# Kernel optimization log

Hardware: AMD Instinct MI355X
Metric: run time of the kernel (lower is better)

Reference implementation:

```python
import jax, jax.numpy as jnp
import numpy as np


def setup_inputs() -> dict:
    key = jax.random.key(0)
    kq, kk, kv = jax.random.split(key, 3)
    N, L, H, D = 2, 2048, 16, 64
    Q = jax.random.normal(kq, (N, L, H, D), dtype=jnp.float32)
    K = jax.random.normal(kk, (N, L, H, D), dtype=jnp.float32)
    V = jax.random.normal(kv, (N, L, H, D), dtype=jnp.float32)
    return {"Q": Q, "K": K, "V": V}


def reference(Q, K, V):
    # Q: [N, l_q, H, d], K: [N, l_k, H, d], V: [N, l_k, H, d_v]
    d_key = K.shape[-1]
    scale = 1.0 / jnp.sqrt(jnp.asarray(d_key, dtype=Q.dtype))
    # scores: [N, l_q, l_k, H] (matches torch sum over d, softmax over l_k)
    scores = jnp.einsum("nqhd,nkhd->nqkh", Q, K) * scale
    attn = jax.nn.softmax(scores, axis=2)
    # out: [N, l_q, H, d_v]
    out = jnp.einsum("nqkh,nkhd->nqhd", attn, V)
    return out
```

## Files before the change

kernel.cpp:

```cpp
#include <hip/hip_runtime.h>
#include <hip/hip_bf16.h>

typedef __attribute__((ext_vector_type(8))) short bf16x8;
typedef __attribute__((ext_vector_type(4))) float float4_t;
typedef __attribute__((ext_vector_type(2))) float f32x2;
typedef __attribute__((ext_vector_type(16))) float f32x16;
typedef __attribute__((ext_vector_type(4))) int int4v;
typedef __attribute__((ext_vector_type(2))) int int2v;

constexpr int Lseq = 2048;
constexpr int ROWS = 1024;
constexpr float SCALE_LOG2E = 0.18033688011112042f;

__device__ short g_Kb[32 * 32 * 4096];
__device__ short g_Vb[32 * 32 * 4096];

__device__ __forceinline__ int cvtpk(float lo, float hi) {
  int r; asm("v_cvt_pk_bf16_f32 %0, %1, %2" : "=v"(r) : "v"(lo), "v"(hi)); return r;
}
__device__ __forceinline__ void plswap(int& a, int& b) {
  int2v r = __builtin_amdgcn_permlane32_swap(a, b, false, false);
  a = r[0]; b = r[1];
}
__device__ __forceinline__ int4v pk8(float4_t a, float4_t b) {
  int4v t;
  t[0] = cvtpk(a[0], a[1]); t[1] = cvtpk(a[2], a[3]);
  t[2] = cvtpk(b[0], b[1]); t[3] = cvtpk(b[2], b[3]);
  return t;
}
__device__ __forceinline__ void dma16(const void* g, void* l) {
  __builtin_amdgcn_global_load_lds(
      (const __attribute__((address_space(1))) void*)g,
      (__attribute__((address_space(3))) void*)l, 16, 0, 0);
}
__device__ __forceinline__ void wait8() {
  asm volatile("s_waitcnt vmcnt(8)" ::: "memory");
  __builtin_amdgcn_sched_barrier(0);
}
__device__ __forceinline__ void wait0() {
  asm volatile("s_waitcnt vmcnt(0)" ::: "memory");
  __builtin_amdgcn_sched_barrier(0);
}

#define MFMA32(A, B, C) __builtin_amdgcn_mfma_f32_32x32x16_bf16((A), (B), (C), 0, 0, 0)

__global__ __launch_bounds__(256)
void preconv(const float* __restrict__ Kg, const float* __restrict__ Vg) {
  const int bid = blockIdx.x;
  const int nh = bid >> 5;
  const int kt = bid & 31;
  const size_t base = (size_t)(nh >> 4) * Lseq * ROWS + (size_t)(nh & 15) * 64;
  const int tid = threadIdx.x;
  char* kimg = (char*)g_Kb + ((size_t)nh * 32 + kt) * 8192;
  char* vimg = (char*)g_Vb + ((size_t)nh * 32 + kt) * 8192;

#pragma unroll
  for (int p = 0; p < 2; ++p) {
    const int f    = tid + p * 256;
    const int half = f >> 8;
    const int c    = (f >> 6) & 3;
    const int hi   = (f >> 5) & 1;
    const int lq   = f & 31;
    {
      const float* src = Kg + base + (size_t)(kt * 64 + half * 32 + lq) * ROWS
                         + c * 16 + hi * 8;
      float4_t a = *(const float4_t*)src;
      float4_t b = *(const float4_t*)(src + 4);
      *(int4v*)(kimg + f * 16) = pk8(a, b);
    }
    {
      const float* src = Vg + base + (size_t)(kt * 64 + c * 16 + hi * 8) * ROWS
                         + half * 32 + lq;
      float v[8];
#pragma unroll
      for (int j = 0; j < 8; ++j) v[j] = src[(size_t)j * ROWS];
      int4v w;
      w[0] = cvtpk(v[0], v[1]); w[1] = cvtpk(v[2], v[3]);
      w[2] = cvtpk(v[4], v[5]); w[3] = cvtpk(v[6], v[7]);
      *(int4v*)(vimg + f * 16) = w;
    }
  }
}

__global__ __launch_bounds__(256, 2)
void attn_fwd(const float* __restrict__ Qg, float* __restrict__ Og) {
  __shared__ __align__(16) short kv[2][4][4096];

  const int wg  = blockIdx.x;
  const int swz = (wg & 7) * 64 + (wg >> 3);
  const int nh  = swz >> 4;
  const int qb  = swz & 15;
  const size_t base = (size_t)(nh >> 4) * Lseq * ROWS + (size_t)(nh & 15) * 64;

  const int tid  = threadIdx.x;
  const int lane = tid & 63;
  const int wid  = tid >> 6;
  const int lq   = lane & 31;
  const int hi   = lane >> 5;

  bf16x8 qf[4];
  {
    const float* qa = Qg + base + (size_t)(qb * 128 + wid * 32 + lq) * ROWS + hi * 8;
#pragma unroll
    for (int c = 0; c < 4; ++c) {
      float4_t a = *(const float4_t*)(qa + c * 16);
      float4_t b = *(const float4_t*)(qa + c * 16 + 4);
#pragma unroll
      for (int j = 0; j < 4; ++j) { a[j] *= SCALE_LOG2E; b[j] *= SCALE_LOG2E; }
      qf[c] = __builtin_bit_cast(bf16x8, pk8(a, b));
    }
  }
  wait0();

  bf16x8 onesf;
#pragma unroll
  for (int j = 0; j < 8; ++j) onesf[j] = (short)0x3F80;

  const char* gimg = ((wid < 2) ? (const char*)g_Kb : (const char*)g_Vb)
                     + (size_t)nh * 262144 + (size_t)(wid & 1) * 8192 + lane * 16;
  auto stage = [&](int buf, int t) {
    const char* s = gimg + (size_t)t * 16384;
    char* d = (char*)&kv[buf][wid][0];
#pragma unroll
    for (int i = 0; i < 8; ++i) dma16(s + i * 1024, d + i * 1024);
  };

  stage(0, 0);
  stage(1, 1);

  f32x16 acc0 = {}, acc1 = {}, lacc = {};
  bf16x8 pa[4];

  auto softmax_pa = [&](f32x16& s0, f32x16& s1) {
#pragma unroll
    for (int r = 0; r < 16; ++r) {
      s0[r] = __builtin_amdgcn_exp2f(s0[r]);
      s1[r] = __builtin_amdgcn_exp2f(s1[r]);
    }
#pragma unroll
    for (int c = 0; c < 4; ++c) {
      const f32x16& sv = (c < 2) ? s0 : s1;
      const int br = (c & 1) * 8;
      int t0 = cvtpk(sv[br + 0], sv[br + 1]);
      int t1 = cvtpk(sv[br + 2], sv[br + 3]);
      int t2 = cvtpk(sv[br + 4], sv[br + 5]);
      int t3 = cvtpk(sv[br + 6], sv[br + 7]);
      plswap(t0, t2);
      plswap(t1, t3);
      int4v tt; tt[0] = t0; tt[1] = t1; tt[2] = t2; tt[3] = t3;
      pa[c] = __builtin_bit_cast(bf16x8, tt);
    }
  };

#pragma unroll 1
  for (int t = 0; t < 16; ++t) {
    wait8();
    __builtin_amdgcn_s_barrier();
    __builtin_amdgcn_sched_barrier(0);

    const int buf = t & 1;
#pragma unroll
    for (int s = 0; s < 2; ++s) {
      const char* kld = (const char*)&kv[buf][s][0]     + lane * 16;
      const char* vld = (const char*)&kv[buf][2 + s][0] + lane * 16;
      f32x16 s0 = {}, s1 = {};
#pragma unroll
      for (int c = 0; c < 4; ++c) {
        s0 = MFMA32(*(const bf16x8*)(kld + c * 1024),        qf[c], s0);
        s1 = MFMA32(*(const bf16x8*)(kld + 4096 + c * 1024), qf[c], s1);
      }
      softmax_pa(s0, s1);
#pragma unroll
      for (int c = 0; c < 4; ++c) {
        acc0 = MFMA32(pa[c], *(const bf16x8*)(vld + c * 1024),        acc0);
        acc1 = MFMA32(pa[c], *(const bf16x8*)(vld + 4096 + c * 1024), acc1);
        lacc = MFMA32(pa[c], onesf, lacc);
      }
    }

    __builtin_amdgcn_sched_barrier(0);
    __builtin_amdgcn_s_barrier();
    stage(buf, (t + 2) & 15);
  }
  wait0();

#pragma unroll
  for (int r = 0; r < 16; ++r) {
    int qr = (r & 3) + 8 * (r >> 2) + 4 * hi;
    const float li = 1.0f / lacc[r];
    float* orow = Og + base + (size_t)(qb * 128 + wid * 32 + qr) * ROWS;
    orow[lq]      = acc0[r] * li;
    orow[32 + lq] = acc1[r] * li;
  }
}

extern "C" void kernel_launch(void* const* d_in, const int* in_sizes, int n_in,
                              void* d_out, int out_size, void* d_ws, size_t ws_size,
                              hipStream_t stream) {
  const float* Q = (const float*)d_in[0];
  const float* K = (const float*)d_in[1];
  const float* V = (const float*)d_in[2];
  float* O = (float*)d_out;
  preconv<<<dim3(1024), dim3(256), 0, stream>>>(K, V);
  attn_fwd<<<dim3(512), dim3(256), 0, stream>>>(Q, O);
}
```

Before: 57.18 us.

## Split key range across warp pairs with 64-row query blocks and LDS merge

Each workgroup now covers 64 query rows instead of 128, and the grid doubles to 1024 blocks. The four waves form two query halves times two key halves, and each key half processes 32 smaller K/V tiles with its own double buffer. Partial outputs and row sums from the second key half are merged through LDS at the end, and LDS per block is halved so launch bounds allow four blocks per CU. This aims to raise occupancy and fill the GPU better, at the cost of an extra reduction step, twice the per-block Q loading, and more barriers per unit of work.

```diff
diff --git a/kernel.cpp b/kernel.cpp
--- a/kernel.cpp
+++ b/kernel.cpp
@@ -3,7 +3,6 @@
 
 typedef __attribute__((ext_vector_type(8))) short bf16x8;
 typedef __attribute__((ext_vector_type(4))) float float4_t;
-typedef __attribute__((ext_vector_type(2))) float f32x2;
 typedef __attribute__((ext_vector_type(16))) float f32x16;
 typedef __attribute__((ext_vector_type(4))) int int4v;
 typedef __attribute__((ext_vector_type(2))) int int2v;
@@ -33,8 +32,8 @@
       (const __attribute__((address_space(1))) void*)g,
       (__attribute__((address_space(3))) void*)l, 16, 0, 0);
 }
-__device__ __forceinline__ void wait8() {
-  asm volatile("s_waitcnt vmcnt(8)" ::: "memory");
+__device__ __forceinline__ void wait4() {
+  asm volatile("s_waitcnt vmcnt(4)" ::: "memory");
   __builtin_amdgcn_sched_barrier(0);
 }
 __device__ __forceinline__ void wait0() {
@@ -82,25 +81,27 @@
   }
 }
 
-__global__ __launch_bounds__(256, 2)
+__global__ __launch_bounds__(256, 4)
 void attn_fwd(const float* __restrict__ Qg, float* __restrict__ Og) {
-  __shared__ __align__(16) short kv[2][4][4096];
+  __shared__ __align__(16) short kv[2][2][2][2048];
 
   const int wg  = blockIdx.x;
-  const int swz = (wg & 7) * 64 + (wg >> 3);
-  const int nh  = swz >> 4;
-  const int qb  = swz & 15;
+  const int swz = (wg & 7) * 128 + (wg >> 3);
+  const int nh  = swz >> 5;
+  const int qb  = swz & 31;
   const size_t base = (size_t)(nh >> 4) * Lseq * ROWS + (size_t)(nh & 15) * 64;
 
   const int tid  = threadIdx.x;
   const int lane = tid & 63;
   const int wid  = tid >> 6;
+  const int p    = wid & 1;
+  const int h    = wid >> 1;
   const int lq   = lane & 31;
   const int hi   = lane >> 5;
 
   bf16x8 qf[4];
   {
-    const float* qa = Qg + base + (size_t)(qb * 128 + wid * 32 + lq) * ROWS + hi * 8;
+    const float* qa = Qg + base + (size_t)(qb * 64 + p * 32 + lq) * ROWS + hi * 8;
 #pragma unroll
     for (int c = 0; c < 4; ++c) {
       float4_t a = *(const float4_t*)(qa + c * 16);
@@ -116,81 +117,94 @@
 #pragma unroll
   for (int j = 0; j < 8; ++j) onesf[j] = (short)0x3F80;
 
-  const char* gimg = ((wid < 2) ? (const char*)g_Kb : (const char*)g_Vb)
-                     + (size_t)nh * 262144 + (size_t)(wid & 1) * 8192 + lane * 16;
-  auto stage = [&](int buf, int t) {
-    const char* s = gimg + (size_t)t * 16384;
-    char* d = (char*)&kv[buf][wid][0];
-#pragma unroll
-    for (int i = 0; i < 8; ++i) dma16(s + i * 1024, d + i * 1024);
+  const char* kimg = (const char*)g_Kb + (size_t)nh * 262144;
+  const char* vimg = (const char*)g_Vb + (size_t)nh * 262144;
+
+  auto stage = [&](int b, int t) {
+    char* d = (char*)&kv[h][b][p][0];
+    const size_t st = (size_t)(h * 16 + (t >> 1)) * 8192;
+    if (p == 0) {
+      const char* s = kimg + st + (t & 1) * 4096 + lane * 16;
+#pragma unroll
+      for (int i = 0; i < 4; ++i) dma16(s + i * 1024, d + i * 1024);
+    } else {
+      const char* s = vimg + st + (t & 1) * 2048 + lane * 16;
+      dma16(s,               d);
+      dma16(s + 1024,        d + 1024);
+      dma16(s + 4096,        d + 2048);
+      dma16(s + 4096 + 1024, d + 3072);
+    }
   };
 
   stage(0, 0);
   stage(1, 1);
 
   f32x16 acc0 = {}, acc1 = {}, lacc = {};
-  bf16x8 pa[4];
-
-  auto softmax_pa = [&](f32x16& s0, f32x16& s1) {
-#pragma unroll
-    for (int r = 0; r < 16; ++r) {
-      s0[r] = __builtin_amdgcn_exp2f(s0[r]);
-      s1[r] = __builtin_amdgcn_exp2f(s1[r]);
-    }
-#pragma unroll
-    for (int c = 0; c < 4; ++c) {
-      const f32x16& sv = (c < 2) ? s0 : s1;
-      const int br = (c & 1) * 8;
-      int t0 = cvtpk(sv[br + 0], sv[br + 1]);
-      int t1 = cvtpk(sv[br + 2], sv[br + 3]);
-      int t2 = cvtpk(sv[br + 4], sv[br + 5]);
-      int t3 = cvtpk(sv[br + 6], sv[br + 7]);
+
+#pragma unroll 1
+  for (int t = 0; t < 32; ++t) {
+    wait4();
+    __builtin_amdgcn_s_barrier();
+    __builtin_amdgcn_sched_barrier(0);
+
+    const int buf = t & 1;
+    const char* kld = (const char*)&kv[h][buf][0][0] + lane * 16;
+    const char* vld = (const char*)&kv[h][buf][1][0] + lane * 16;
+
+    f32x16 s = {};
+#pragma unroll
+    for (int c = 0; c < 4; ++c)
+      s = MFMA32(*(const bf16x8*)(kld + c * 1024), qf[c], s);
+
+#pragma unroll
+    for (int r = 0; r < 16; ++r) s[r] = __builtin_amdgcn_exp2f(s[r]);
+    bf16x8 pa[2];
+#pragma unroll
+    for (int c = 0; c < 2; ++c) {
+      const int br = c * 8;
+      int t0 = cvtpk(s[br + 0], s[br + 1]);
+      int t1 = cvtpk(s[br + 2], s[br + 3]);
+      int t2 = cvtpk(s[br + 4], s[br + 5]);
+      int t3 = cvtpk(s[br + 6], s[br + 7]);
       plswap(t0, t2);
       plswap(t1, t3);
       int4v tt; tt[0] = t0; tt[1] = t1; tt[2] = t2; tt[3] = t3;
       pa[c] = __builtin_bit_cast(bf16x8, tt);
     }
-  };
-
-#pragma unroll 1
-  for (int t = 0; t < 16; ++t) {
-    wait8();
-    __builtin_amdgcn_s_barrier();
-    __builtin_amdgcn_sched_barrier(0);
-
-    const int buf = t & 1;
-#pragma unroll
-    for (int s = 0; s < 2; ++s) {
-      const char* kld = (const char*)&kv[buf][s][0]     + lane * 16;
-      const char* vld = (const char*)&kv[buf][2 + s][0] + lane * 16;
-      f32x16 s0 = {}, s1 = {};
-#pragma unroll
-      for (int c = 0; c < 4; ++c) {
-        s0 = MFMA32(*(const bf16x8*)(kld + c * 1024),        qf[c], s0);
-        s1 = MFMA32(*(const bf16x8*)(kld + 4096 + c * 1024), qf[c], s1);
-      }
-      softmax_pa(s0, s1);
-#pragma unroll
-      for (int c = 0; c < 4; ++c) {
-        acc0 = MFMA32(pa[c], *(const bf16x8*)(vld + c * 1024),        acc0);
-        acc1 = MFMA32(pa[c], *(const bf16x8*)(vld + 4096 + c * 1024), acc1);
-        lacc = MFMA32(pa[c], onesf, lacc);
-      }
+
+#pragma unroll
+    for (int ks = 0; ks < 2; ++ks) {
+      acc0 = MFMA32(pa[ks], *(const bf16x8*)(vld + ks * 1024),        acc0);
+      acc1 = MFMA32(pa[ks], *(const bf16x8*)(vld + 2048 + ks * 1024), acc1);
+      lacc = MFMA32(pa[ks], onesf, lacc);
     }
 
     __builtin_amdgcn_sched_barrier(0);
     __builtin_amdgcn_s_barrier();
-    stage(buf, (t + 2) & 15);
+    stage(buf, (t + 2) & 31);
   }
   wait0();
-
-#pragma unroll
-  for (int r = 0; r < 16; ++r) {
-    int qr = (r & 3) + 8 * (r >> 2) + 4 * hi;
-    const float li = 1.0f / lacc[r];
-    float* orow = Og + base + (size_t)(qb * 128 + wid * 32 + qr) * ROWS;
-    orow[lq]      = acc0[r] * li;
-    orow[32 + lq] = acc1[r] * li;
+  __builtin_amdgcn_s_barrier();
+
+  float* scr = (float*)&kv[0][0][0][0] + p * 3072 + lane * 48;
+  if (h == 1) {
+#pragma unroll
+    for (int r = 0; r < 16; ++r) {
+      scr[r]      = acc0[r];
+      scr[16 + r] = acc1[r];
+      scr[32 + r] = lacc[r];
+    }
+  }
+  __builtin_amdgcn_s_barrier();
+  if (h == 0) {
+#pragma unroll
+    for (int r = 0; r < 16; ++r) {
+      const int qr = (r & 3) + 8 * (r >> 2) + 4 * hi;
+      const float li = 1.0f / (lacc[r] + scr[32 + r]);
+      float* orow = Og + base + (size_t)(qb * 64 + p * 32 + qr) * ROWS;
+      orow[lq]      = (acc0[r] + scr[r]) * li;
+      orow[32 + lq] = (acc1[r] + scr[16 + r]) * li;
+    }
   }
 }
 
@@ -202,5 +216,5 @@
   const float* V = (const float*)d_in[2];
   float* O = (float*)d_out;
   preconv<<<dim3(1024), dim3(256), 0, stream>>>(K, V);
-  attn_fwd<<<dim3(512), dim3(256), 0, stream>>>(Q, O);
-}
+  attn_fwd<<<dim3(1024), dim3(256), 0, stream>>>(Q, O);
+}
```

Result: slower. 63.61 us (+11.2%).
